# Kernel tuning notes

Hardware: AMD Instinct MI355X
Metric: run time of the kernel (lower is better)

The kernel has to match this reference:

```python
import jax, jax.numpy as jnp
import numpy as np


def _combos(n, k):
    # all n-tuples of nonnegative ints summing to k, same order as the torch module
    if n == 1:
        yield (k,)
        return
    for i in range(k + 1):
        for t in _combos(n - 1, k - i):
            yield (i,) + t


def _make_exponents(action_dim, rank):
    rows = []
    for total in range(rank + 1):
        rows.extend(_combos(action_dim, total))
    # [action_dim, num_basis], matching the registered buffer exponents.T layout
    return np.asarray(rows, dtype=np.int32).T


def setup_inputs() -> dict:
    key = jax.random.key(0)
    action_dim, rank, batch = 8, 4, 131072
    actions = jax.random.normal(key, (batch, action_dim), dtype=jnp.float32)
    exponents = jnp.asarray(_make_exponents(action_dim, rank))  # [D, NB], NB=495
    return {"actions": actions, "exponents": exponents, "rank": rank}


def reference(actions, exponents, rank):
    # actions: [B, D] float; exponents: [D, NB] int32; rank: python int
    x = jnp.clip(actions, -1.0, 1.0)  # [B, D]
    # Legendre recurrence P_n(x) = ((2n-1)/n) x P_{n-1}(x) - ((n-1)/n) P_{n-2}(x)
    polys = [jnp.ones_like(x)]
    if rank >= 1:
        polys.append(x)
    for n in range(2, rank + 1):
        polys.append(((2.0 * n - 1.0) / n) * x * polys[-1] - ((n - 1.0) / n) * polys[-2])
    P = jnp.stack(polys, axis=-1)  # [B, D, rank+1]
    # gather the needed order per (dimension, basis function) and multiply over dims
    idx = jnp.broadcast_to(exponents[None, :, :], (x.shape[0],) + exponents.shape)  # [B, D, NB]
    gathered = jnp.take_along_axis(P, idx.astype(jnp.int32), axis=2)  # [B, D, NB]
    return jnp.prod(gathered, axis=1)  # [B, NB]
```

## Files before the change

kernel.cpp:

```cpp
#include <hip/hip_runtime.h>
#include <math.h>


#define THREADS 256
#define TILE 32
#define RSTRIDE 142

typedef float f32x4 __attribute__((ext_vector_type(4)));

__device__ __forceinline__ int c2i(int n){ return (n < 2) ? 0 : (n*(n-1))>>1; }
__device__ __forceinline__ int c3i(int n){ return (n < 3) ? 0 : (n*(n-1)*(n-2))/6; }
__device__ __forceinline__ int c4i(int n){ return (n < 4) ? 0 : (n*(n-1)*(n-2)*(n-3))/24; }

__device__ __forceinline__ int rank4(int a, int b, int c, int d) {
    return (70 - c4i(8-a)) + (c3i(7-a) - c3i(7-a-b))
         + (c2i(6-a-b) - c2i(6-a-b-c)) + d;
}

__global__ __launch_bounds__(THREADS, 4) void legendre_fast(
    const float* __restrict__ actions,
    const int* __restrict__ exps,
    float* __restrict__ out)
{
    __shared__ unsigned long long cprog[495];
    __shared__ float UV[TILE * RSTRIDE];
    __shared__ unsigned short tmp16[496];

    const int t = threadIdx.x;
    const int r0 = blockIdx.x * TILE;

    for (int nb = t; nb < 495; nb += THREADS) {
        int e0 = exps[0*495+nb], e1 = exps[1*495+nb];
        int e2 = exps[2*495+nb], e3 = exps[3*495+nb];
        int e4 = exps[4*495+nb], e5 = exps[5*495+nb];
        int e6 = exps[6*495+nb], e7 = exps[7*495+nb];
        int ai = rank4(e0, e1, e2, e3);
        int bi = rank4(e4, e5, e6, e7);
        tmp16[nb] = (unsigned short)(ai | (bi << 7));
    }
    __syncthreads();

    if (t < 64) {
        int row = t >> 1, half = t & 1;
        f32x4 xv = *(const f32x4*)(actions + (long long)(r0 + row) * 8 + half * 4);
        float P[4][5];
#pragma unroll
        for (int d = 0; d < 4; ++d) {
            float x = fminf(fmaxf(xv[d], -1.0f), 1.0f);
            P[d][0] = 1.0f; P[d][1] = x;
#pragma unroll
            for (int n = 2; n <= 4; ++n) {
                float fn = (float)n;
                P[d][n] = ((2.0f*fn - 1.0f)/fn) * x * P[d][n-1]
                        - ((fn - 1.0f)/fn) * P[d][n-2];
            }
        }
        float* W = &UV[row * RSTRIDE + half * 71];
        int cnt = 0;
#pragma unroll
        for (int a = 0; a <= 4; ++a) { float q0 = P[0][a];
#pragma unroll
            for (int b = 0; b <= 4-a; ++b) { float q1 = q0 * P[1][b];
#pragma unroll
                for (int c = 0; c <= 4-a-b; ++c) { float q2 = q1 * P[2][c];
#pragma unroll
                    for (int d = 0; d <= 4-a-b-c; ++d) { W[cnt++] = q2 * P[3][d]; }
                }
            }
        }
    } else {
        for (int j = t - 64; j < 495; j += THREADS - 64) {
            int f = 4 * j;
            int nb0 = f;
            nb0 -= (nb0 >= 990) ? 990 : 0;
            nb0 -= (nb0 >= 495) ? 495 : 0;
            unsigned p0 = tmp16[nb0];
            int n1 = nb0 + 1; unsigned w1 = (n1 >= 495); n1 -= w1 ? 495 : 0;
            int n2 = nb0 + 2; unsigned w2 = (n2 >= 495); n2 -= w2 ? 495 : 0;
            int n3 = nb0 + 3; unsigned w3 = (n3 >= 495); n3 -= w3 ? 495 : 0;
            unsigned p1 = tmp16[n1], p2 = tmp16[n2], p3 = tmp16[n3];
            unsigned lo = p0 | (p1 << 14) | (w1 << 28) | (w2 << 29) | (w3 << 30);
            unsigned hi = p2 | (p3 << 14);
            cprog[j] = ((unsigned long long)hi << 32) | lo;
        }
    }
    __syncthreads();

    const int nchunks = TILE * 495 / 4;
    f32x4* __restrict__ o4 = (f32x4*)(out + (long long)r0 * 495);

    int m = t;
    int f0 = 4 * t;
    int rl = (f0 >= 495) + (f0 >= 990);
    int nb0 = f0 - rl * 495;
    int rowoff = rl * RSTRIDE;

    for (int c = t; c < nchunks; c += THREADS) {
        unsigned long long e = cprog[m];
        unsigned lo = (unsigned)e, hi = (unsigned)(e >> 32);
        float r0v, r1v, r2v, r3v;
        {
            int a = lo & 127, b = (lo >> 7) & 127;
            r0v = UV[rowoff + a] * UV[rowoff + 71 + b];
        }
        {
            int a = (lo >> 14) & 127, b = (lo >> 21) & 127;
            int ro = rowoff + (((lo >> 28) & 1) ? RSTRIDE : 0);
            r1v = UV[ro + a] * UV[ro + 71 + b];
        }
        {
            int a = hi & 127, b = (hi >> 7) & 127;
            int ro = rowoff + (((lo >> 29) & 1) ? RSTRIDE : 0);
            r2v = UV[ro + a] * UV[ro + 71 + b];
        }
        {
            int a = (hi >> 14) & 127, b = (hi >> 21) & 127;
            int ro = rowoff + (((lo >> 30) & 1) ? RSTRIDE : 0);
            r3v = UV[ro + a] * UV[ro + 71 + b];
        }
        f32x4 v; v.x = r0v; v.y = r1v; v.z = r2v; v.w = r3v;
        o4[c] = v;

        m += THREADS; if (m >= 495) m -= 495;
        nb0 += 34; rowoff += 2 * RSTRIDE;
        if (nb0 >= 495) { nb0 -= 495; rowoff += RSTRIDE; }
    }
}

__global__ void legendre_generic(
    const float* __restrict__ actions,
    const int* __restrict__ exps,
    float* __restrict__ out,
    long long total, int D, int NB)
{
    long long stride = (long long)gridDim.x * blockDim.x;
    for (long long i = (long long)blockIdx.x * blockDim.x + threadIdx.x;
         i < total; i += stride) {
        int nb = (int)(i % NB);
        long long row = i / NB;
        float prod = 1.0f;
        for (int d = 0; d < D; ++d) {
            int e = exps[d * NB + nb];
            float x = actions[row * D + d];
            x = fminf(fmaxf(x, -1.0f), 1.0f);
            float p0 = 1.0f, p1 = x;
            float p = (e == 0) ? 1.0f : x;
            for (int n = 2; n <= e; ++n) {
                float fn = (float)n;
                float pn = ((2.0f*fn - 1.0f)/fn) * x * p1 - ((fn - 1.0f)/fn) * p0;
                p0 = p1; p1 = pn; p = pn;
            }
            prod *= p;
        }
        out[i] = prod;
    }
}

extern "C" void kernel_launch(void* const* d_in, const int* in_sizes, int n_in,
                              void* d_out, int out_size, void* d_ws, size_t ws_size,
                              hipStream_t stream) {
    const float* actions = (const float*)d_in[0];
    const int* exps = (const int*)d_in[1];
    float* out = (float*)d_out;

    long long in0 = in_sizes[0];
    long long in1 = in_sizes[1];
    long long osz = out_size;

    int D = (int)(sqrt((double)in0 * (double)in1 / (double)osz) + 0.5);
    if (D < 1) D = 1;
    int NB = (int)(in1 / D);
    int B = (int)(in0 / D);

    bool fast = (D == 8 && NB == 495 &&
                 (long long)B * NB == osz && (long long)B * D == in0 &&
                 (B % TILE) == 0);

    if (fast) {
        legendre_fast<<<B / TILE, THREADS, 0, stream>>>(actions, exps, out);
    } else {
        long long total = osz;
        long long want = (total + 255) / 256;
        int nblk = (want > 8192) ? 8192 : (int)(want > 0 ? want : 1);
        legendre_generic<<<nblk, 256, 0, stream>>>(
            actions, exps, out, total, D, NB);
    }
}
```

Baseline: 46.90 us.

## Transpose half-products in LDS and assign one basis column per thread

Stores the two 70-entry half-product tables transposed, indexed by basis half then row, so each thread owns one basis function. The thread keeps its two table indices in registers and reads four rows at a time with vector LDS loads. This removes the packed chunk program, its extra LDS table and one barrier, and doubles the tile to 64 rows with 512 threads. The trade is that global stores become scalar per thread with a 495-float row stride instead of 16-byte vector stores. Writes stay coalesced across the threads of a row, but the number of store instructions goes up.

```diff
diff --git a/kernel.cpp b/kernel.cpp
--- a/kernel.cpp
+++ b/kernel.cpp
@@ -2,9 +2,9 @@
 #include <math.h>
 
 
-#define THREADS 256
-#define TILE 32
-#define RSTRIDE 142
+#define THREADS 512
+#define TILE 64
+#define TSTR 68
 
 typedef float f32x4 __attribute__((ext_vector_type(4)));
 
@@ -17,30 +17,28 @@
          + (c2i(6-a-b) - c2i(6-a-b-c)) + d;
 }
 
-__global__ __launch_bounds__(THREADS, 4) void legendre_fast(
+__global__ __launch_bounds__(THREADS, 8) void legendre_fast(
     const float* __restrict__ actions,
     const int* __restrict__ exps,
     float* __restrict__ out)
 {
-    __shared__ unsigned long long cprog[495];
-    __shared__ float UV[TILE * RSTRIDE];
-    __shared__ unsigned short tmp16[496];
+    __shared__ float UT[70 * TSTR];
+    __shared__ float VT[70 * TSTR];
 
     const int t = threadIdx.x;
     const int r0 = blockIdx.x * TILE;
 
-    for (int nb = t; nb < 495; nb += THREADS) {
-        int e0 = exps[0*495+nb], e1 = exps[1*495+nb];
-        int e2 = exps[2*495+nb], e3 = exps[3*495+nb];
-        int e4 = exps[4*495+nb], e5 = exps[5*495+nb];
-        int e6 = exps[6*495+nb], e7 = exps[7*495+nb];
-        int ai = rank4(e0, e1, e2, e3);
-        int bi = rank4(e4, e5, e6, e7);
-        tmp16[nb] = (unsigned short)(ai | (bi << 7));
+    int ai = 0, bi = 0;
+    if (t < 495) {
+        int e0 = exps[0*495+t], e1 = exps[1*495+t];
+        int e2 = exps[2*495+t], e3 = exps[3*495+t];
+        int e4 = exps[4*495+t], e5 = exps[5*495+t];
+        int e6 = exps[6*495+t], e7 = exps[7*495+t];
+        ai = rank4(e0, e1, e2, e3);
+        bi = rank4(e4, e5, e6, e7);
     }
-    __syncthreads();
 
-    if (t < 64) {
+    if (t < 2 * TILE) {
         int row = t >> 1, half = t & 1;
         f32x4 xv = *(const f32x4*)(actions + (long long)(r0 + row) * 8 + half * 4);
         float P[4][5];
@@ -55,7 +53,7 @@
                         - ((fn - 1.0f)/fn) * P[d][n-2];
             }
         }
-        float* W = &UV[row * RSTRIDE + half * 71];
+        float* W = (half ? VT : UT) + row;
         int cnt = 0;
 #pragma unroll
         for (int a = 0; a <= 4; ++a) { float q0 = P[0][a];
@@ -64,66 +62,30 @@
 #pragma unroll
                 for (int c = 0; c <= 4-a-b; ++c) { float q2 = q1 * P[2][c];
 #pragma unroll
-                    for (int d = 0; d <= 4-a-b-c; ++d) { W[cnt++] = q2 * P[3][d]; }
+                    for (int d = 0; d <= 4-a-b-c; ++d) {
+                        W[cnt * TSTR] = q2 * P[3][d];
+                        ++cnt;
+                    }
                 }
             }
-        }
-    } else {
-        for (int j = t - 64; j < 495; j += THREADS - 64) {
-            int f = 4 * j;
-            int nb0 = f;
-            nb0 -= (nb0 >= 990) ? 990 : 0;
-            nb0 -= (nb0 >= 495) ? 495 : 0;
-            unsigned p0 = tmp16[nb0];
-            int n1 = nb0 + 1; unsigned w1 = (n1 >= 495); n1 -= w1 ? 495 : 0;
-            int n2 = nb0 + 2; unsigned w2 = (n2 >= 495); n2 -= w2 ? 495 : 0;
-            int n3 = nb0 + 3; unsigned w3 = (n3 >= 495); n3 -= w3 ? 495 : 0;
-            unsigned p1 = tmp16[n1], p2 = tmp16[n2], p3 = tmp16[n3];
-            unsigned lo = p0 | (p1 << 14) | (w1 << 28) | (w2 << 29) | (w3 << 30);
-            unsigned hi = p2 | (p3 << 14);
-            cprog[j] = ((unsigned long long)hi << 32) | lo;
         }
     }
     __syncthreads();
 
-    const int nchunks = TILE * 495 / 4;
-    f32x4* __restrict__ o4 = (f32x4*)(out + (long long)r0 * 495);
-
-    int m = t;
-    int f0 = 4 * t;
-    int rl = (f0 >= 495) + (f0 >= 990);
-    int nb0 = f0 - rl * 495;
-    int rowoff = rl * RSTRIDE;
-
-    for (int c = t; c < nchunks; c += THREADS) {
-        unsigned long long e = cprog[m];
-        unsigned lo = (unsigned)e, hi = (unsigned)(e >> 32);
-        float r0v, r1v, r2v, r3v;
-        {
-            int a = lo & 127, b = (lo >> 7) & 127;
-            r0v = UV[rowoff + a] * UV[rowoff + 71 + b];
+    if (t < 495) {
+        const float* Urow = &UT[ai * TSTR];
+        const float* Vrow = &VT[bi * TSTR];
+        float* obase = out + (long long)r0 * 495 + t;
+#pragma unroll 4
+        for (int q = 0; q < TILE / 4; ++q) {
+            f32x4 u = *(const f32x4*)(Urow + 4 * q);
+            f32x4 v = *(const f32x4*)(Vrow + 4 * q);
+            float* o = obase + (long long)(4 * q) * 495;
+            o[0]        = u.x * v.x;
+            o[495]      = u.y * v.y;
+            o[2 * 495]  = u.z * v.z;
+            o[3 * 495]  = u.w * v.w;
         }
-        {
-            int a = (lo >> 14) & 127, b = (lo >> 21) & 127;
-            int ro = rowoff + (((lo >> 28) & 1) ? RSTRIDE : 0);
-            r1v = UV[ro + a] * UV[ro + 71 + b];
-        }
-        {
-            int a = hi & 127, b = (hi >> 7) & 127;
-            int ro = rowoff + (((lo >> 29) & 1) ? RSTRIDE : 0);
-            r2v = UV[ro + a] * UV[ro + 71 + b];
-        }
-        {
-            int a = (hi >> 14) & 127, b = (hi >> 21) & 127;
-            int ro = rowoff + (((lo >> 30) & 1) ? RSTRIDE : 0);
-            r3v = UV[ro + a] * UV[ro + 71 + b];
-        }
-        f32x4 v; v.x = r0v; v.y = r1v; v.z = r2v; v.w = r3v;
-        o4[c] = v;
-
-        m += THREADS; if (m >= 495) m -= 495;
-        nb0 += 34; rowoff += 2 * RSTRIDE;
-        if (nb0 >= 495) { nb0 -= 495; rowoff += RSTRIDE; }
     }
 }
 
```

Result: no change. 47.09 us (median of 2 runs) (+0.4%).
